# Kernel tuning notes

Measured on AMD Instinct MI355X. Metric: run time of the kernel, lower is better.

The kernel has to match this reference:

```python
import jax, jax.numpy as jnp
import numpy as np

B, S = 128, 400
EMB, ENC, DEC = 128, 1024, 300
VOCAB, MAX_OOV = 50000, 50


def setup_inputs() -> dict:
    key = jax.random.key(0)
    ks = jax.random.split(key, 16)
    s = 0.05
    return {
        "embedded": jax.random.normal(ks[0], (B, EMB), jnp.float32),
        "enc_output": jax.random.normal(ks[1], (B, S, ENC), jnp.float32),
        "h1": jax.random.normal(ks[2], (B, DEC), jnp.float32),
        "pad_mask": jnp.zeros((B, S), jnp.bool_),
        "max_n_oov": MAX_OOV,
        "source_WORD_encoding_extended": jax.random.randint(ks[3], (B, S), 0, VOCAB + MAX_OOV),
        # parameters
        "W_attn1": jax.random.normal(ks[4], (ENC, DEC), jnp.float32) * s,
        "W_attn2": jax.random.normal(ks[5], (ENC, DEC), jnp.float32) * s,
        "W_ih": jax.random.normal(ks[6], (3 * DEC, EMB + ENC), jnp.float32) * s,
        "W_hh": jax.random.normal(ks[7], (3 * DEC, DEC), jnp.float32) * s,
        "b_ih": jax.random.normal(ks[8], (3 * DEC,), jnp.float32) * s,
        "b_hh": jax.random.normal(ks[9], (3 * DEC,), jnp.float32) * s,
        "W_out": jax.random.normal(ks[10], (VOCAB, ENC + DEC), jnp.float32) * s,
        "b_out": jax.random.normal(ks[11], (VOCAB,), jnp.float32) * s,
        "W_p": jax.random.normal(ks[12], (1, ENC + DEC), jnp.float32) * s,
        "b_p": jax.random.normal(ks[13], (1,), jnp.float32) * s,
    }


def _additive_attn(h, enc_output, W, pad_mask):
    # h: [B, DEC], enc_output: [B, S, ENC], W: [ENC, DEC]
    e = jnp.einsum('bse,ed->bsd', enc_output, W)
    scores = jnp.einsum('bd,bsd->bs', h, e)
    scores = jnp.where(pad_mask, -jnp.inf, scores)
    return jax.nn.softmax(scores, axis=1)  # [B, S]


def _gru_cell(x, h, W_ih, W_hh, b_ih, b_hh):
    gx = x @ W_ih.T + b_ih  # [B, 3*DEC]
    gh = h @ W_hh.T + b_hh
    xr, xz, xn = jnp.split(gx, 3, axis=1)
    hr, hz, hn = jnp.split(gh, 3, axis=1)
    r = jax.nn.sigmoid(xr + hr)
    z = jax.nn.sigmoid(xz + hz)
    n = jnp.tanh(xn + r * hn)
    return (1.0 - z) * n + z * h


def reference(embedded, enc_output, h1, pad_mask, max_n_oov,
              source_WORD_encoding_extended, W_attn1, W_attn2,
              W_ih, W_hh, b_ih, b_hh, W_out, b_out, W_p, b_p):
    a = _additive_attn(h1, enc_output, W_attn1, pad_mask)
    weighted = jnp.einsum('bs,bse->be', a, enc_output)
    rnn_input = jnp.concatenate([embedded, weighted], axis=1)
    h_new = _gru_cell(rnn_input, h1, W_ih, W_hh, b_ih, b_hh)

    a2 = _additive_attn(h_new, enc_output, W_attn2, pad_mask)
    weighted2 = jnp.einsum('bs,bse->be', a2, enc_output)
    hw = jnp.concatenate([h_new, weighted2], axis=1)  # [B, DEC+ENC]

    p_vocab = jax.nn.softmax(hw @ W_out.T + b_out, axis=1)  # [B, VOCAB]
    p_gen = jax.nn.sigmoid(hw @ W_p.T + b_p)  # [B, 1]

    bsz = p_vocab.shape[0]
    ext_zeros = jnp.zeros((bsz, max_n_oov), p_vocab.dtype)
    p_out = p_gen * jnp.concatenate([p_vocab, ext_zeros], axis=1)
    rows = jnp.arange(bsz)[:, None]
    p_out = p_out.at[rows, source_WORD_encoding_extended].add((1.0 - p_gen) * a2)
    return p_out, h_new
```

## Files before the change

kernel.cpp:

```cpp
#include <hip/hip_runtime.h>
#include <stdint.h>

constexpr int B_     = 128;
constexpr int S_     = 400;
constexpr int EMB_   = 128;
constexpr int ENC_   = 1024;
constexpr int DEC_   = 300;
constexpr int VOCAB_ = 50000;
constexpr int OOV_   = 50;
constexpr int OUTW_  = VOCAB_ + OOV_;
constexpr int KHW_   = ENC_ + DEC_;
constexpr int KHWP_  = 1344;
constexpr int G3_    = 3 * DEC_;
constexpr int KIN_   = EMB_ + ENC_;
constexpr int CHK_   = 96;
constexpr int CHKB_  = 192;
constexpr int NC_    = 14;
constexpr int PSTRIDE_ = 1028;
constexpr int NTILE_ = 782;

typedef __attribute__((ext_vector_type(4))) float f32x4;
typedef __attribute__((ext_vector_type(8))) short short8;

__device__ __forceinline__ float dot4(float4 a, float4 b) {
  return a.x * b.x + a.y * b.y + a.z * b.z + a.w * b.w;
}

__device__ __forceinline__ short f2bf(float f) {
  uint32_t u = __builtin_bit_cast(uint32_t, f);
  u += 0x7fffu + ((u >> 16) & 1u);
  return (short)(u >> 16);
}

__global__ __launch_bounds__(256) void k_compute_v(const float* __restrict__ W,
                                                   const float* __restrict__ h,
                                                   float* __restrict__ v) {
  int b = blockIdx.x;
  __shared__ __align__(16) float hs[DEC_];
  for (int d = threadIdx.x; d < DEC_; d += 256) hs[d] = h[b * DEC_ + d];
  __syncthreads();
  for (int e = threadIdx.x; e < ENC_; e += 256) {
    const float4* w4 = (const float4*)(W + (size_t)e * DEC_);
    const float4* h4 = (const float4*)hs;
    float acc = 0.f;
    #pragma unroll 5
    for (int d = 0; d < DEC_ / 4; ++d) acc += dot4(w4[d], h4[d]);
    v[b * ENC_ + e] = acc;
  }
}

__global__ __launch_bounds__(256) void k_attn_pass(const float* __restrict__ enc,
                                                   const float* __restrict__ v,
                                                   float* __restrict__ scores,
                                                   float* __restrict__ part, int nsplit) {
  int b = blockIdx.x, split = blockIdx.y;
  int wave = threadIdx.x >> 6, lane = threadIdx.x & 63;
  float4 vr[4];
  #pragma unroll
  for (int c = 0; c < 4; ++c) vr[c] = *(const float4*)(v + b * ENC_ + c * 256 + lane * 4);
  float m = -INFINITY, l = 0.f;
  float4 wa[4];
  #pragma unroll
  for (int c = 0; c < 4; ++c) wa[c] = make_float4(0.f, 0.f, 0.f, 0.f);
  int rows = S_ / nsplit, s0 = split * rows, s_end = s0 + rows;
  int s = s0 + wave;
  for (; s + 4 < s_end; s += 8) {
    const float* era = enc + ((size_t)b * S_ + s) * ENC_;
    const float* erb = enc + ((size_t)b * S_ + s + 4) * ENC_;
    float4 e4a[4], e4b[4];
    #pragma unroll
    for (int c = 0; c < 4; ++c) {
      e4a[c] = *(const float4*)(era + c * 256 + lane * 4);
      e4b[c] = *(const float4*)(erb + c * 256 + lane * 4);
    }
    float pa = 0.f, pb = 0.f;
    #pragma unroll
    for (int c = 0; c < 4; ++c) { pa += dot4(e4a[c], vr[c]); pb += dot4(e4b[c], vr[c]); }
    #pragma unroll
    for (int off = 32; off; off >>= 1) {
      pa += __shfl_xor(pa, off);
      pb += __shfl_xor(pb, off);
    }
    if (lane == 0) { scores[b * S_ + s] = pa; scores[b * S_ + s + 4] = pb; }
    float nm = fmaxf(m, fmaxf(pa, pb));
    float sc = __expf(m - nm);
    float ea = __expf(pa - nm);
    float eb = __expf(pb - nm);
    l = l * sc + ea + eb;
    #pragma unroll
    for (int c = 0; c < 4; ++c) {
      wa[c].x = wa[c].x * sc + ea * e4a[c].x + eb * e4b[c].x;
      wa[c].y = wa[c].y * sc + ea * e4a[c].y + eb * e4b[c].y;
      wa[c].z = wa[c].z * sc + ea * e4a[c].z + eb * e4b[c].z;
      wa[c].w = wa[c].w * sc + ea * e4a[c].w + eb * e4b[c].w;
    }
    m = nm;
  }
  if (s < s_end) {
    const float* er = enc + ((size_t)b * S_ + s) * ENC_;
    float4 e4[4];
    #pragma unroll
    for (int c = 0; c < 4; ++c) e4[c] = *(const float4*)(er + c * 256 + lane * 4);
    float p = 0.f;
    #pragma unroll
    for (int c = 0; c < 4; ++c) p += dot4(e4[c], vr[c]);
    #pragma unroll
    for (int off = 32; off; off >>= 1) p += __shfl_xor(p, off);
    if (lane == 0) scores[b * S_ + s] = p;
    float nm = fmaxf(m, p);
    float sc = __expf(m - nm), pe = __expf(p - nm);
    l = l * sc + pe;
    #pragma unroll
    for (int c = 0; c < 4; ++c) {
      wa[c].x = wa[c].x * sc + pe * e4[c].x;
      wa[c].y = wa[c].y * sc + pe * e4[c].y;
      wa[c].z = wa[c].z * sc + pe * e4[c].z;
      wa[c].w = wa[c].w * sc + pe * e4[c].w;
    }
    m = nm;
  }
  float* pp = part + ((size_t)b * (nsplit * 4) + split * 4 + wave) * PSTRIDE_;
  #pragma unroll
  for (int c = 0; c < 4; ++c) *(float4*)(pp + c * 256 + lane * 4) = wa[c];
  if (lane == 0) { pp[1024] = m; pp[1025] = l; }
}

__global__ __launch_bounds__(256) void k_attn_merge1(const float* __restrict__ part, int P,
                                                     float* __restrict__ wout) {
  int b = blockIdx.x, tid = threadIdx.x;
  const float* pb = part + (size_t)b * P * PSTRIDE_;
  __shared__ float scl[32];
  __shared__ float Ls;
  if (tid == 0) {
    float M = -INFINITY;
    for (int p = 0; p < P; ++p) M = fmaxf(M, pb[p * PSTRIDE_ + 1024]);
    float L = 0.f;
    for (int p = 0; p < P; ++p) {
      float lp = pb[p * PSTRIDE_ + 1025];
      float e = (lp > 0.f) ? __expf(pb[p * PSTRIDE_ + 1024] - M) : 0.f;
      scl[p] = e;
      L += lp * e;
    }
    Ls = L;
  }
  __syncthreads();
  float invL = 1.f / Ls;
  for (int e = tid; e < ENC_; e += 256) {
    float acc = 0.f;
    for (int p = 0; p < P; ++p) acc += scl[p] * pb[p * PSTRIDE_ + e];
    wout[(size_t)b * ENC_ + e] = acc * invL;
  }
}

__global__ __launch_bounds__(256) void k_attn_merge2(const float* __restrict__ part, int P,
                                                     short* __restrict__ hwb,
                                                     float* __restrict__ ml,
                                                     const float* __restrict__ W_p,
                                                     const float* __restrict__ b_p,
                                                     const float* __restrict__ pg_acc,
                                                     float* __restrict__ pg) {
  int b = blockIdx.x, tid = threadIdx.x;
  const float* pb = part + (size_t)b * P * PSTRIDE_;
  __shared__ float scl[32];
  __shared__ float Ls;
  __shared__ float red[256];
  if (tid == 0) {
    float M = -INFINITY;
    for (int p = 0; p < P; ++p) M = fmaxf(M, pb[p * PSTRIDE_ + 1024]);
    float L = 0.f;
    for (int p = 0; p < P; ++p) {
      float lp = pb[p * PSTRIDE_ + 1025];
      float e = (lp > 0.f) ? __expf(pb[p * PSTRIDE_ + 1024] - M) : 0.f;
      scl[p] = e;
      L += lp * e;
    }
    Ls = L;
    ml[b * 2] = M; ml[b * 2 + 1] = L;
  }
  __syncthreads();
  float invL = 1.f / Ls;
  float pacc = 0.f;
  for (int e = tid; e < ENC_; e += 256) {
    float acc = 0.f;
    for (int p = 0; p < P; ++p) acc += scl[p] * pb[p * PSTRIDE_ + e];
    float w = acc * invL;
    hwb[(size_t)b * KHWP_ + DEC_ + e] = f2bf(w);
    pacc += w * W_p[DEC_ + e];
  }
  if (tid < KHWP_ - KHW_) hwb[(size_t)b * KHWP_ + KHW_ + tid] = 0;
  red[tid] = pacc;
  __syncthreads();
  for (int st = 128; st > 0; st >>= 1) {
    if (tid < st) red[tid] += red[tid + st];
    __syncthreads();
  }
  if (tid == 0) pg[b] = 1.f / (1.f + __expf(-(red[0] + pg_acc[b] + b_p[0])));
}

__global__ __launch_bounds__(256) void k_gates(const float* __restrict__ emb,
                                               const float* __restrict__ wgt,
                                               const float* __restrict__ h1,
                                               const float* __restrict__ W_ih,
                                               const float* __restrict__ W_hh,
                                               const float* __restrict__ b_ih,
                                               const float* __restrict__ b_hh,
                                               float* __restrict__ gx, float* __restrict__ gh,
                                               float* __restrict__ pg_acc) {
  int idx = blockIdx.x * 256 + threadIdx.x;
  if (idx < B_) pg_acc[idx] = 0.f;
  int b = idx & (B_ - 1);
  int g = idx >> 7;
  if (g >= G3_) return;
  const float4* wr = (const float4*)(W_ih + (size_t)g * KIN_);
  const float4* xe = (const float4*)(emb + b * EMB_);
  const float4* xw = (const float4*)(wgt + b * ENC_);
  float accx = b_ih[g];
  #pragma unroll 8
  for (int k = 0; k < EMB_ / 4; ++k) accx += dot4(wr[k], xe[k]);
  #pragma unroll 8
  for (int k = 0; k < ENC_ / 4; ++k) accx += dot4(wr[EMB_ / 4 + k], xw[k]);
  const float4* wh = (const float4*)(W_hh + (size_t)g * DEC_);
  const float4* xh = (const float4*)(h1 + b * DEC_);
  float acch = b_hh[g];
  #pragma unroll 5
  for (int k = 0; k < DEC_ / 4; ++k) acch += dot4(wh[k], xh[k]);
  gx[g * B_ + b] = accx;
  gh[g * B_ + b] = acch;
}

__global__ __launch_bounds__(256) void k_gru_combine(const float* __restrict__ gx,
                                                     const float* __restrict__ gh,
                                                     const float* __restrict__ h1,
                                                     float* __restrict__ hn,
                                                     short* __restrict__ hwb,
                                                     float* __restrict__ outh,
                                                     const float* __restrict__ W_p,
                                                     float* __restrict__ pg_acc) {
  int j = blockIdx.x * 256 + threadIdx.x;
  int b = blockIdx.y;
  __shared__ float red[256];
  float pp = 0.f;
  if (j < DEC_) {
    float xr = gx[j * B_ + b], xz = gx[(j + DEC_) * B_ + b], xn = gx[(j + 2 * DEC_) * B_ + b];
    float hr = gh[j * B_ + b], hz = gh[(j + DEC_) * B_ + b], hnn = gh[(j + 2 * DEC_) * B_ + b];
    float r = 1.f / (1.f + __expf(-(xr + hr)));
    float z = 1.f / (1.f + __expf(-(xz + hz)));
    float n = tanhf(xn + r * hnn);
    float h = (1.f - z) * n + z * h1[b * DEC_ + j];
    hn[b * DEC_ + j] = h;
    hwb[(size_t)b * KHWP_ + j] = f2bf(h);
    outh[b * DEC_ + j] = h;
    pp = h * W_p[j];
  }
  red[threadIdx.x] = pp;
  __syncthreads();
  for (int st = 128; st > 0; st >>= 1) {
    if (threadIdx.x < st) red[threadIdx.x] += red[threadIdx.x + st];
    __syncthreads();
  }
  if (threadIdx.x == 0) atomicAdd(pg_acc + b, red[0]);
}

__global__ __launch_bounds__(256) void k_outproj(const short* __restrict__ A,
                                                 const float* __restrict__ Wo,
                                                 const float* __restrict__ bo,
                                                 float* __restrict__ out,
                                                 float* __restrict__ pml) {
  __shared__ __align__(16) short A_lds[2 * B_ * CHK_];
  int tid = threadIdx.x;
  int wave = tid >> 6, lane = tid & 63;
  int r16 = lane & 15, kg = lane >> 4;
  int vcol = blockIdx.x * 64 + wave * 16 + r16;
  int vload = vcol < VOCAB_ ? vcol : VOCAB_ - 1;
  const float* brow = Wo + (size_t)vload * KHW_ + kg * 8;
  f32x4 acc[8];
  #pragma unroll
  for (int mi = 0; mi < 8; ++mi) acc[mi] = (f32x4){0.f, 0.f, 0.f, 0.f};

  const char* A8 = (const char*)A;
  uint32_t srcoff[6];
  #pragma unroll
  for (int i = 0; i < 6; ++i) {
    int g = tid + i * 256;
    int row = g / 12, j = g % 12;
    int bp = j >> 2, tp = j & 3;
    int bl = (bp + 3 - row % 3) % 3;
    int tl_ = tp ^ (row & 3);
    srcoff[i] = (uint32_t)(row * 2688 + bl * 64 + tl_ * 16);
  }
  int rm3 = r16 % 3;
  int rot0 = rm3 * 64;
  int rot1 = ((rm3 + 1) % 3) * 64;
  int rot2 = ((rm3 + 2) % 3) * 64;
  int slotoff = (kg ^ (r16 & 3)) << 4;

  float4 br[2][6];
  float  tl[8];

  #pragma unroll
  for (int i = 0; i < 6; ++i)
    __builtin_amdgcn_global_load_lds(
        (const __attribute__((address_space(1))) void*)(A8 + srcoff[i]),
        (__attribute__((address_space(3))) void*)((char*)A_lds + i * 4096 + wave * 1024),
        16, 0, 0);
  #pragma unroll
  for (int s = 0; s < 3; ++s) {
    br[0][2 * s]     = *(const float4*)(brow + s * 32);
    br[0][2 * s + 1] = *(const float4*)(brow + s * 32 + 4);
  }

  #pragma unroll
  for (int c = 0; c < NC_; ++c) {
    __syncthreads();
    if (c < NC_ - 1) {
      char* dstb = (char*)A_lds + ((c + 1) & 1) * 24576;
      #pragma unroll
      for (int i = 0; i < 6; ++i)
        __builtin_amdgcn_global_load_lds(
            (const __attribute__((address_space(1))) void*)(A8 + srcoff[i] + (c + 1) * CHKB_),
            (__attribute__((address_space(3))) void*)(dstb + i * 4096 + wave * 1024),
            16, 0, 0);
      if (c + 1 < NC_ - 1) {
        #pragma unroll
        for (int s = 0; s < 3; ++s) {
          br[(c + 1) & 1][2 * s]     = *(const float4*)(brow + (c + 1) * CHK_ + s * 32);
          br[(c + 1) & 1][2 * s + 1] = *(const float4*)(brow + (c + 1) * CHK_ + s * 32 + 4);
        }
      } else {
        #pragma unroll
        for (int s = 0; s < 2; ++s) {
          br[(c + 1) & 1][2 * s]     = *(const float4*)(brow + 13 * CHK_ + s * 32);
          br[(c + 1) & 1][2 * s + 1] = *(const float4*)(brow + 13 * CHK_ + s * 32 + 4);
        }
        #pragma unroll
        for (int j = 0; j < 8; ++j)
          tl[j] = (kg * 8 + j < KHW_ - 1312) ? brow[1312 + j] : 0.f;
      }
    }
    const char* rbase = (const char*)A_lds + (c & 1) * 24576 + r16 * CHKB_;
    #pragma unroll
    for (int s = 0; s < 3; ++s) {
      short8 bf;
      if (c == NC_ - 1 && s == 2) {
        #pragma unroll
        for (int j = 0; j < 8; ++j) bf[j] = f2bf(tl[j]);
      } else {
        float4 b0 = br[c & 1][2 * s], b1 = br[c & 1][2 * s + 1];
        bf[0] = f2bf(b0.x); bf[1] = f2bf(b0.y); bf[2] = f2bf(b0.z); bf[3] = f2bf(b0.w);
        bf[4] = f2bf(b1.x); bf[5] = f2bf(b1.y); bf[6] = f2bf(b1.z); bf[7] = f2bf(b1.w);
      }
      #pragma unroll
      for (int mi = 0; mi < 8; ++mi) {
        int t = (s + mi) % 3;
        int blkoff = (t == 0) ? rot0 : ((t == 1) ? rot1 : rot2);
        short8 af = *(const short8*)(rbase + mi * 3072 + blkoff + slotoff);
        acc[mi] = __builtin_amdgcn_mfma_f32_16x16x32_bf16(af, bf, acc[mi], 0, 0, 0);
      }
    }
  }

  __syncthreads();
  float* wml = (float*)A_lds;

  bool valid = vcol < VOCAB_;
  float biasv = bo[vload];
  #pragma unroll
  for (int mi = 0; mi < 8; ++mi) {
    #pragma unroll
    for (int j = 0; j < 4; ++j) {
      float lv = valid ? acc[mi][j] + biasv : -INFINITY;
      if (valid) out[(size_t)(mi * 16 + kg * 4 + j) * OUTW_ + vcol] = lv;
      float mr = lv;
      #pragma unroll
      for (int msk = 1; msk < 16; msk <<= 1) mr = fmaxf(mr, __shfl_xor(mr, msk));
      float se = valid ? __expf(lv - mr) : 0.f;
      #pragma unroll
      for (int msk = 1; msk < 16; msk <<= 1) se += __shfl_xor(se, msk);
      if (r16 == 0) {
        wml[(wave * B_ + mi * 16 + kg * 4 + j) * 2]     = mr;
        wml[(wave * B_ + mi * 16 + kg * 4 + j) * 2 + 1] = se;
      }
    }
  }
  __syncthreads();
  if (tid < B_) {
    float M = -INFINITY;
    #pragma unroll
    for (int w = 0; w < 4; ++w) M = fmaxf(M, wml[(w * B_ + tid) * 2]);
    float L = 0.f;
    #pragma unroll
    for (int w = 0; w < 4; ++w) {
      float lw = wml[(w * B_ + tid) * 2 + 1];
      if (lw > 0.f) L += lw * __expf(wml[(w * B_ + tid) * 2] - M);
    }
    pml[((size_t)blockIdx.x * B_ + tid) * 2]     = M;
    pml[((size_t)blockIdx.x * B_ + tid) * 2 + 1] = L;
  }
}

__global__ __launch_bounds__(256) void k_vfinal(float* __restrict__ out,
                                                const float* __restrict__ pml,
                                                const float* __restrict__ pg,
                                                float* __restrict__ mlv) {
  int bq = blockIdx.x, b = blockIdx.y, t = threadIdx.x;
  __shared__ float rm[256], rl[256];
  float lm = -INFINITY, ll = 0.f;
  for (int tile = t; tile < NTILE_; tile += 256) {
    float m = pml[((size_t)tile * B_ + b) * 2];
    float l = pml[((size_t)tile * B_ + b) * 2 + 1];
    float M = fmaxf(lm, m);
    float nl = 0.f;
    if (ll > 0.f) nl += ll * __expf(lm - M);
    if (l > 0.f) nl += l * __expf(m - M);
    lm = M; ll = nl;
  }
  rm[t] = lm; rl[t] = ll;
  __syncthreads();
  for (int st = 128; st > 0; st >>= 1) {
    if (t < st) {
      float m1 = rm[t], l1 = rl[t], m2 = rm[t + st], l2 = rl[t + st];
      float M = fmaxf(m1, m2);
      float L = (l1 > 0.f ? l1 * __expf(m1 - M) : 0.f) + (l2 > 0.f ? l2 * __expf(m2 - M) : 0.f);
      rm[t] = M; rl[t] = L;
    }
    __syncthreads();
  }
  float M = rm[0], L = rl[0];
  float scale = pg[b] / L;
  float* row = out + (size_t)b * OUTW_;
  int lo = bq * 12513;
  int hi = min(lo + 12513, OUTW_);
  for (int v = lo + t; v < hi; v += 256)
    row[v] = (v < VOCAB_) ? scale * __expf(row[v] - M) : 0.f;
  if (bq == 0 && t == 0) { mlv[b * 2] = M; mlv[b * 2 + 1] = L; }
}

__global__ __launch_bounds__(256) void k_scatter2(float* __restrict__ out,
                                                  const int* __restrict__ src,
                                                  const float* __restrict__ scores,
                                                  const float* __restrict__ ml2,
                                                  const float* __restrict__ pg) {
  int b = blockIdx.x, t = threadIdx.x;
  float M2 = ml2[b * 2], L2 = ml2[b * 2 + 1];
  float q = (1.f - pg[b]) / L2;
  float* row = out + (size_t)b * OUTW_;
  for (int s = t; s < S_; s += 256) {
    float val = q * __expf(scores[b * S_ + s] - M2);
    atomicAdd(row + src[b * S_ + s], val);
  }
}

extern "C" void kernel_launch(void* const* d_in, const int* in_sizes, int n_in,
                              void* d_out, int out_size, void* d_ws, size_t ws_size,
                              hipStream_t stream) {
  const float* embedded = (const float*)d_in[0];
  const float* enc      = (const float*)d_in[1];
  const float* h1       = (const float*)d_in[2];
  const int*   src      = (const int*)d_in[5];
  const float* W1       = (const float*)d_in[6];
  const float* W2       = (const float*)d_in[7];
  const float* W_ih     = (const float*)d_in[8];
  const float* W_hh     = (const float*)d_in[9];
  const float* b_ih     = (const float*)d_in[10];
  const float* b_hh     = (const float*)d_in[11];
  const float* W_out    = (const float*)d_in[12];
  const float* b_out    = (const float*)d_in[13];
  const float* W_p      = (const float*)d_in[14];
  const float* b_p      = (const float*)d_in[15];
  float* out = (float*)d_out;
  float* ws  = (float*)d_ws;

  size_t off = 0;
  float* v_ws    = ws + off; off += (size_t)B_ * ENC_;
  float* w1_ws   = ws + off; off += (size_t)B_ * ENC_;
  float* gx_ws   = ws + off; off += (size_t)G3_ * B_;
  float* gh_ws   = ws + off; off += (size_t)G3_ * B_;
  float* hn_ws   = ws + off; off += (size_t)B_ * DEC_;
  float* sc_ws   = ws + off; off += (size_t)B_ * S_;
  float* ml2_ws  = ws + off; off += 256;
  float* pg_ws   = ws + off; off += 128;
  float* pga_ws  = ws + off; off += 128;
  float* mlv_ws  = ws + off; off += 256;
  float* pml_ws  = ws + off; off += (size_t)NTILE_ * B_ * 2;
  short* hwb_ws  = (short*)(ws + off); off += (size_t)B_ * KHWP_ / 2;
  float* part_ws = ws + off;

  int NS = 8;
  while (NS > 1 && (off + (size_t)B_ * NS * 4 * PSTRIDE_) * 4 > ws_size) NS >>= 1;

  k_compute_v<<<B_, 256, 0, stream>>>(W1, h1, v_ws);
  k_attn_pass<<<dim3(B_, NS), 256, 0, stream>>>(enc, v_ws, sc_ws, part_ws, NS);
  k_attn_merge1<<<B_, 256, 0, stream>>>(part_ws, NS * 4, w1_ws);
  k_gates<<<(G3_ * B_) / 256, 256, 0, stream>>>(embedded, w1_ws, h1, W_ih, W_hh, b_ih, b_hh,
                                                gx_ws, gh_ws, pga_ws);
  k_gru_combine<<<dim3(2, B_), 256, 0, stream>>>(gx_ws, gh_ws, h1, hn_ws, hwb_ws,
                                                 out + (size_t)B_ * OUTW_, W_p, pga_ws);
  k_compute_v<<<B_, 256, 0, stream>>>(W2, hn_ws, v_ws);
  k_attn_pass<<<dim3(B_, NS), 256, 0, stream>>>(enc, v_ws, sc_ws, part_ws, NS);
  k_attn_merge2<<<B_, 256, 0, stream>>>(part_ws, NS * 4, hwb_ws, ml2_ws, W_p, b_p,
                                        pga_ws, pg_ws);
  k_outproj<<<NTILE_, 256, 0, stream>>>(hwb_ws, W_out, b_out, out, pml_ws);
  k_vfinal<<<dim3(4, B_), 256, 0, stream>>>(out, pml_ws, pg_ws, mlv_ws);
  k_scatter2<<<B_, 256, 0, stream>>>(out, src, sc_ws, ml2_ws, pg_ws);
}
```

Before: 443.8 us.

## Shrink outproj K-chunk with XOR swizzle, fuse scatter into vfinal, parallelize merges

The output-projection GEMM now uses 64-wide K chunks (21 stages) with a simple XOR-swizzled LDS layout, replacing the 96-wide rotated layout. This lowers LDS use and address math, at the cost of more pipeline stages and barriers. The serial thread-0 softmax merge in both attention merge kernels becomes a wave-wide shuffle reduction, and the attention split count doubles to 16. The scatter kernel is folded into k_vfinal, where each block adds only the indices in its own vocab range, saving a launch.

```diff
diff --git a/kernel.cpp b/kernel.cpp
--- a/kernel.cpp
+++ b/kernel.cpp
@@ -13,9 +13,9 @@
 constexpr int KHWP_  = 1344;
 constexpr int G3_    = 3 * DEC_;
 constexpr int KIN_   = EMB_ + ENC_;
-constexpr int CHK_   = 96;
-constexpr int CHKB_  = 192;
-constexpr int NC_    = 14;
+constexpr int CHK_   = 64;
+constexpr int CHKB_  = 128;
+constexpr int NC_    = 21;
 constexpr int PSTRIDE_ = 1028;
 constexpr int NTILE_ = 782;
 
@@ -129,19 +129,20 @@
                                                      float* __restrict__ wout) {
   int b = blockIdx.x, tid = threadIdx.x;
   const float* pb = part + (size_t)b * P * PSTRIDE_;
-  __shared__ float scl[32];
+  __shared__ float scl[64];
   __shared__ float Ls;
-  if (tid == 0) {
-    float M = -INFINITY;
-    for (int p = 0; p < P; ++p) M = fmaxf(M, pb[p * PSTRIDE_ + 1024]);
-    float L = 0.f;
-    for (int p = 0; p < P; ++p) {
-      float lp = pb[p * PSTRIDE_ + 1025];
-      float e = (lp > 0.f) ? __expf(pb[p * PSTRIDE_ + 1024] - M) : 0.f;
-      scl[p] = e;
-      L += lp * e;
-    }
-    Ls = L;
+  if (tid < 64) {
+    float mp = (tid < P) ? pb[tid * PSTRIDE_ + 1024] : -INFINITY;
+    float lp = (tid < P) ? pb[tid * PSTRIDE_ + 1025] : 0.f;
+    float M = mp;
+    #pragma unroll
+    for (int off = 32; off; off >>= 1) M = fmaxf(M, __shfl_xor(M, off));
+    float e = (lp > 0.f) ? __expf(mp - M) : 0.f;
+    scl[tid] = e;
+    float Lc = lp * e;
+    #pragma unroll
+    for (int off = 32; off; off >>= 1) Lc += __shfl_xor(Lc, off);
+    if (tid == 0) Ls = Lc;
   }
   __syncthreads();
   float invL = 1.f / Ls;
@@ -161,21 +162,21 @@
                                                      float* __restrict__ pg) {
   int b = blockIdx.x, tid = threadIdx.x;
   const float* pb = part + (size_t)b * P * PSTRIDE_;
-  __shared__ float scl[32];
+  __shared__ float scl[64];
   __shared__ float Ls;
   __shared__ float red[256];
-  if (tid == 0) {
-    float M = -INFINITY;
-    for (int p = 0; p < P; ++p) M = fmaxf(M, pb[p * PSTRIDE_ + 1024]);
-    float L = 0.f;
-    for (int p = 0; p < P; ++p) {
-      float lp = pb[p * PSTRIDE_ + 1025];
-      float e = (lp > 0.f) ? __expf(pb[p * PSTRIDE_ + 1024] - M) : 0.f;
-      scl[p] = e;
-      L += lp * e;
-    }
-    Ls = L;
-    ml[b * 2] = M; ml[b * 2 + 1] = L;
+  if (tid < 64) {
+    float mp = (tid < P) ? pb[tid * PSTRIDE_ + 1024] : -INFINITY;
+    float lp = (tid < P) ? pb[tid * PSTRIDE_ + 1025] : 0.f;
+    float M = mp;
+    #pragma unroll
+    for (int off = 32; off; off >>= 1) M = fmaxf(M, __shfl_xor(M, off));
+    float e = (lp > 0.f) ? __expf(mp - M) : 0.f;
+    scl[tid] = e;
+    float Lc = lp * e;
+    #pragma unroll
+    for (int off = 32; off; off >>= 1) Lc += __shfl_xor(Lc, off);
+    if (tid == 0) { Ls = Lc; ml[b * 2] = M; ml[b * 2 + 1] = Lc; }
   }
   __syncthreads();
   float invL = 1.f / Ls;
@@ -278,33 +279,26 @@
   for (int mi = 0; mi < 8; ++mi) acc[mi] = (f32x4){0.f, 0.f, 0.f, 0.f};
 
   const char* A8 = (const char*)A;
-  uint32_t srcoff[6];
-  #pragma unroll
-  for (int i = 0; i < 6; ++i) {
+  uint32_t srcoff[4];
+  #pragma unroll
+  for (int i = 0; i < 4; ++i) {
     int g = tid + i * 256;
-    int row = g / 12, j = g % 12;
-    int bp = j >> 2, tp = j & 3;
-    int bl = (bp + 3 - row % 3) % 3;
-    int tl_ = tp ^ (row & 3);
-    srcoff[i] = (uint32_t)(row * 2688 + bl * 64 + tl_ * 16);
-  }
-  int rm3 = r16 % 3;
-  int rot0 = rm3 * 64;
-  int rot1 = ((rm3 + 1) % 3) * 64;
-  int rot2 = ((rm3 + 2) % 3) * 64;
-  int slotoff = (kg ^ (r16 & 3)) << 4;
-
-  float4 br[2][6];
+    int row = g >> 3, sp = g & 7;
+    int sl = sp ^ (row & 7);
+    srcoff[i] = (uint32_t)(row * 2688 + sl * 16);
+  }
+
+  float4 br[2][4];
   float  tl[8];
 
   #pragma unroll
-  for (int i = 0; i < 6; ++i)
+  for (int i = 0; i < 4; ++i)
     __builtin_amdgcn_global_load_lds(
         (const __attribute__((address_space(1))) void*)(A8 + srcoff[i]),
         (__attribute__((address_space(3))) void*)((char*)A_lds + i * 4096 + wave * 1024),
         16, 0, 0);
   #pragma unroll
-  for (int s = 0; s < 3; ++s) {
+  for (int s = 0; s < 2; ++s) {
     br[0][2 * s]     = *(const float4*)(brow + s * 32);
     br[0][2 * s + 1] = *(const float4*)(brow + s * 32 + 4);
   }
@@ -313,35 +307,32 @@
   for (int c = 0; c < NC_; ++c) {
     __syncthreads();
     if (c < NC_ - 1) {
-      char* dstb = (char*)A_lds + ((c + 1) & 1) * 24576;
+      char* dstb = (char*)A_lds + ((c + 1) & 1) * 16384;
       #pragma unroll
-      for (int i = 0; i < 6; ++i)
+      for (int i = 0; i < 4; ++i)
         __builtin_amdgcn_global_load_lds(
             (const __attribute__((address_space(1))) void*)(A8 + srcoff[i] + (c + 1) * CHKB_),
             (__attribute__((address_space(3))) void*)(dstb + i * 4096 + wave * 1024),
             16, 0, 0);
       if (c + 1 < NC_ - 1) {
         #pragma unroll
-        for (int s = 0; s < 3; ++s) {
+        for (int s = 0; s < 2; ++s) {
           br[(c + 1) & 1][2 * s]     = *(const float4*)(brow + (c + 1) * CHK_ + s * 32);
           br[(c + 1) & 1][2 * s + 1] = *(const float4*)(brow + (c + 1) * CHK_ + s * 32 + 4);
         }
       } else {
-        #pragma unroll
-        for (int s = 0; s < 2; ++s) {
-          br[(c + 1) & 1][2 * s]     = *(const float4*)(brow + 13 * CHK_ + s * 32);
-          br[(c + 1) & 1][2 * s + 1] = *(const float4*)(brow + 13 * CHK_ + s * 32 + 4);
-        }
+        br[0][0] = *(const float4*)(brow + 20 * CHK_);
+        br[0][1] = *(const float4*)(brow + 20 * CHK_ + 4);
         #pragma unroll
         for (int j = 0; j < 8; ++j)
           tl[j] = (kg * 8 + j < KHW_ - 1312) ? brow[1312 + j] : 0.f;
       }
     }
-    const char* rbase = (const char*)A_lds + (c & 1) * 24576 + r16 * CHKB_;
-    #pragma unroll
-    for (int s = 0; s < 3; ++s) {
+    const char* rbase = (const char*)A_lds + (c & 1) * 16384 + r16 * CHKB_;
+    #pragma unroll
+    for (int s = 0; s < 2; ++s) {
       short8 bf;
-      if (c == NC_ - 1 && s == 2) {
+      if (c == NC_ - 1 && s == 1) {
         #pragma unroll
         for (int j = 0; j < 8; ++j) bf[j] = f2bf(tl[j]);
       } else {
@@ -349,11 +340,10 @@
         bf[0] = f2bf(b0.x); bf[1] = f2bf(b0.y); bf[2] = f2bf(b0.z); bf[3] = f2bf(b0.w);
         bf[4] = f2bf(b1.x); bf[5] = f2bf(b1.y); bf[6] = f2bf(b1.z); bf[7] = f2bf(b1.w);
       }
+      int sl = ((s << 2) + kg) ^ (r16 & 7);
       #pragma unroll
       for (int mi = 0; mi < 8; ++mi) {
-        int t = (s + mi) % 3;
-        int blkoff = (t == 0) ? rot0 : ((t == 1) ? rot1 : rot2);
-        short8 af = *(const short8*)(rbase + mi * 3072 + blkoff + slotoff);
+        short8 af = *(const short8*)(rbase + mi * 2048 + (sl << 4));
         acc[mi] = __builtin_amdgcn_mfma_f32_16x16x32_bf16(af, bf, acc[mi], 0, 0, 0);
       }
     }
@@ -401,7 +391,9 @@
 __global__ __launch_bounds__(256) void k_vfinal(float* __restrict__ out,
                                                 const float* __restrict__ pml,
                                                 const float* __restrict__ pg,
-                                                float* __restrict__ mlv) {
+                                                const int* __restrict__ src,
+                                                const float* __restrict__ scores,
+                                                const float* __restrict__ ml2) {
   int bq = blockIdx.x, b = blockIdx.y, t = threadIdx.x;
   __shared__ float rm[256], rl[256];
   float lm = -INFINITY, ll = 0.f;
@@ -426,27 +418,21 @@
     __syncthreads();
   }
   float M = rm[0], L = rl[0];
-  float scale = pg[b] / L;
+  float p = pg[b];
+  float scale = p / L;
   float* row = out + (size_t)b * OUTW_;
   int lo = bq * 12513;
   int hi = min(lo + 12513, OUTW_);
   for (int v = lo + t; v < hi; v += 256)
     row[v] = (v < VOCAB_) ? scale * __expf(row[v] - M) : 0.f;
-  if (bq == 0 && t == 0) { mlv[b * 2] = M; mlv[b * 2 + 1] = L; }
-}
-
-__global__ __launch_bounds__(256) void k_scatter2(float* __restrict__ out,
-                                                  const int* __restrict__ src,
-                                                  const float* __restrict__ scores,
-                                                  const float* __restrict__ ml2,
-                                                  const float* __restrict__ pg) {
-  int b = blockIdx.x, t = threadIdx.x;
+  __syncthreads();
   float M2 = ml2[b * 2], L2 = ml2[b * 2 + 1];
-  float q = (1.f - pg[b]) / L2;
-  float* row = out + (size_t)b * OUTW_;
+  float q = (1.f - p) / L2;
   for (int s = t; s < S_; s += 256) {
-    float val = q * __expf(scores[b * S_ + s] - M2);
-    atomicAdd(row + src[b * S_ + s], val);
+    int cidx = src[b * S_ + s];
+    if (cidx >= lo && cidx < hi) {
+      atomicAdd(row + cidx, q * __expf(scores[b * S_ + s] - M2));
+    }
   }
 }
 
@@ -480,12 +466,11 @@
   float* ml2_ws  = ws + off; off += 256;
   float* pg_ws   = ws + off; off += 128;
   float* pga_ws  = ws + off; off += 128;
-  float* mlv_ws  = ws + off; off += 256;
   float* pml_ws  = ws + off; off += (size_t)NTILE_ * B_ * 2;
   short* hwb_ws  = (short*)(ws + off); off += (size_t)B_ * KHWP_ / 2;
   float* part_ws = ws + off;
 
-  int NS = 8;
+  int NS = 16;
   while (NS > 1 && (off + (size_t)B_ * NS * 4 * PSTRIDE_) * 4 > ws_size) NS >>= 1;
 
   k_compute_v<<<B_, 256, 0, stream>>>(W1, h1, v_ws);
@@ -500,6 +485,5 @@
   k_attn_merge2<<<B_, 256, 0, stream>>>(part_ws, NS * 4, hwb_ws, ml2_ws, W_p, b_p,
                                         pga_ws, pg_ws);
   k_outproj<<<NTILE_, 256, 0, stream>>>(hwb_ws, W_out, b_out, out, pml_ws);
-  k_vfinal<<<dim3(4, B_), 256, 0, stream>>>(out, pml_ws, pg_ws, mlv_ws);
-  k_scatter2<<<B_, 256, 0, stream>>>(out, src, sc_ws, ml2_ws, pg_ws);
-}
+  k_vfinal<<<dim3(4, B_), 256, 0, stream>>>(out, pml_ws, pg_ws, src, sc_ws, ml2_ws);
+}
```

Measured after the change: 453.3 us. 1.02x slower.
